# Kernel optimization log

Hardware: AMD Instinct MI355X
Metric: run time of the kernel (lower is better)

Reference implementation:

```python
import jax, jax.numpy as jnp
import numpy as np

B, C, N, K = 8, 256, 4096, 16

def setup_inputs() -> dict:
    key = jax.random.key(0)
    k1, k2, k3 = jax.random.split(key, 3)
    x = jax.random.normal(k1, (B, C, N, 1), dtype=jnp.float32)
    edge_index = jax.random.randint(k2, (2, B, N, K), 0, N, dtype=jnp.int64)
    eps = jnp.zeros((1,), dtype=jnp.float32)
    W = jax.random.normal(k3, (C, C), dtype=jnp.float32) * (1.0 / np.sqrt(C))
    b = jnp.zeros((C,), dtype=jnp.float32)
    return {"x": x, "edge_index": edge_index, "eps": eps, "W": W, "b": b}

def reference(x, edge_index, eps, W, b):
    # x: [B, C, N, 1]; edge_index: [2, B, N, K]
    idx = edge_index[0]                                  # [B, N, K] neighbor ids
    x_sq = x[..., 0]                                     # [B, C, N]
    # batched_index_select: gather neighbor features -> [B, C, N, K]
    gath = jnp.take_along_axis(
        x_sq, idx.reshape(B, 1, N * K).astype(jnp.int32), axis=2
    ).reshape(B, C, N, K)
    x_j = jnp.sum(gath, axis=-1, keepdims=True)          # [B, C, N, 1]
    h = (1.0 + eps[0]) * x + x_j                         # GIN update
    # BasicConv: 1x1 Conv2d + bias + ReLU
    out = jnp.einsum('oc,bcnk->bonk', W, h) + b[None, :, None, None]
    return jax.nn.relu(out)
```

## Files before the change

### kernel.cpp

```cpp
#include <hip/hip_runtime.h>
#include <stdint.h>

#define BB 8
#define CC 256
#define NN 4096
#define KK 16
#define NT 32

typedef float f32x4 __attribute__((ext_vector_type(4)));
typedef short bf16x8 __attribute__((ext_vector_type(8)));
typedef int   i32x4 __attribute__((ext_vector_type(4)));

__device__ __forceinline__ ushort f2bf(float f) {
  union { float f; uint32_t u; } v; v.f = f;
  uint32_t r = v.u + 0x7FFFu + ((v.u >> 16) & 1u);
  return (ushort)(r >> 16);
}
__device__ __forceinline__ float bf2f(ushort h) {
  union { uint32_t u; float f; } v; v.u = ((uint32_t)h) << 16;
  return v.f;
}

__global__ __launch_bounds__(256) void k_prep(
    const float* __restrict__ x, const float* __restrict__ W,
    ushort* __restrict__ xT, ushort* __restrict__ Wfrag)
{
  const int bid = blockIdx.x;
  const int t   = threadIdx.x;
  if (bid >= 2048) {
    const int wb = bid - 2048;
    const int o  = wb * 4 + (t >> 6);
    const int k0 = (t & 63) * 4;
    float4 v = *(const float4*)(W + (size_t)o * CC + k0);
    ushort4 h;
    h.x = f2bf(v.x); h.y = f2bf(v.y); h.z = f2bf(v.z); h.w = f2bf(v.w);
    const int kc = k0 >> 5, ks = k0 & 31;
    *(ushort4*)(Wfrag + ((size_t)(kc * CC + o)) * 32 + ks) = h;
    return;
  }
  __shared__ float tile[64][68];
  const int b    = bid & 7;
  const int tl   = bid >> 3;
  const int c0   = (tl & 3) * 64;
  const int n0   = (tl >> 2) * 64;
  {
    const int r  = t >> 2;
    const int cs = (t & 3) * 16;
    const float* xp = x + ((size_t)b * CC + c0 + r) * NN + n0 + cs;
    #pragma unroll
    for (int i = 0; i < 4; ++i) {
      float4 v = *(const float4*)(xp + i * 4);
      *(float4*)&tile[r][cs + i * 4] = v;
    }
  }
  __syncthreads();
  const int nl = t >> 2;
  const int cl = (t & 3) * 16;
  union { ushort s[16]; uint4 q[2]; } pk;
  #pragma unroll
  for (int i = 0; i < 16; ++i) pk.s[i] = f2bf(tile[cl + i][nl]);
  uint4* dst = (uint4*)(xT + ((size_t)b * NN + n0 + nl) * CC + c0 + cl);
  dst[0] = pk.q[0];
  dst[1] = pk.q[1];
}

__global__ __launch_bounds__(256) void k_fused(
    const ushort* __restrict__ xT, const int* __restrict__ edge0,
    const float* __restrict__ eps, const ushort* __restrict__ Wfrag,
    const float* __restrict__ bias, float* __restrict__ out)
{
  __shared__ ushort hLds[NT][264];
  const int bid = blockIdx.x;
  const int b   = bid & 7;
  const int n0  = (bid >> 3) * NT;
  const int t    = threadIdx.x;
  const int wave = t >> 6, lane = t & 63;
  const float epsv = 1.0f + eps[0];
  const ushort* xb = xT + (size_t)b * NN * CC;

  const int half = lane >> 5;
  const int cl   = (lane & 31) * 8;
  #pragma unroll
  for (int it = 0; it < 4; ++it) {
    const int nl = wave * 8 + it * 2 + half;
    const int n  = n0 + nl;
    bf16x8 sv = *(const bf16x8*)(xb + (size_t)n * CC + cl);
    float a[8];
    #pragma unroll
    for (int j = 0; j < 8; ++j) a[j] = bf2f((ushort)sv[j]) * epsv;
    const i32x4* epv = (const i32x4*)(edge0 + ((size_t)b * NN + n) * KK);
    i32x4 e0 = __builtin_nontemporal_load(epv + 0);
    i32x4 e1 = __builtin_nontemporal_load(epv + 1);
    i32x4 e2 = __builtin_nontemporal_load(epv + 2);
    i32x4 e3 = __builtin_nontemporal_load(epv + 3);
    const int js[16] = {e0.x, e0.y, e0.z, e0.w, e1.x, e1.y, e1.z, e1.w,
                        e2.x, e2.y, e2.z, e2.w, e3.x, e3.y, e3.z, e3.w};
    #pragma unroll
    for (int k = 0; k < KK; ++k) {
      bf16x8 g = *(const bf16x8*)(xb + (size_t)js[k] * CC + cl);
      #pragma unroll
      for (int j = 0; j < 8; ++j) a[j] += bf2f((ushort)g[j]);
    }
    union { ushort s[8]; bf16x8 v; } pk;
    #pragma unroll
    for (int j = 0; j < 8; ++j) pk.s[j] = f2bf(a[j]);
    *(bf16x8*)&hLds[nl][cl] = pk.v;
  }
  __syncthreads();

  f32x4 acc[4][NT / 16];
  #pragma unroll
  for (int m = 0; m < 4; ++m)
    #pragma unroll
    for (int nn = 0; nn < NT / 16; ++nn) acc[m][nn] = (f32x4){0.f, 0.f, 0.f, 0.f};

  const int lrow = lane & 15;
  const int kgrp = lane >> 4;
  const int o0   = wave * 64;

  #pragma unroll
  for (int kc = 0; kc < 8; ++kc) {
    const int cs = kgrp * 8;
    bf16x8 afr[4], bfr[NT / 16];
    #pragma unroll
    for (int m = 0; m < 4; ++m)
      afr[m] = *(const bf16x8*)(Wfrag +
          ((size_t)(kc * CC + o0 + m * 16 + lrow)) * 32 + cs);
    #pragma unroll
    for (int nn = 0; nn < NT / 16; ++nn)
      bfr[nn] = *(const bf16x8*)&hLds[nn * 16 + lrow][kc * 32 + cs];
    #pragma unroll
    for (int m = 0; m < 4; ++m)
      #pragma unroll
      for (int nn = 0; nn < NT / 16; ++nn)
        acc[m][nn] = __builtin_amdgcn_mfma_f32_16x16x32_bf16(
            afr[m], bfr[nn], acc[m][nn], 0, 0, 0);
  }

  #pragma unroll
  for (int m = 0; m < 4; ++m) {
    #pragma unroll
    for (int r = 0; r < 4; ++r) {
      const int o  = o0 + m * 16 + kgrp * 4 + r;
      const float bv = bias[o];
      #pragma unroll
      for (int nn = 0; nn < NT / 16; ++nn) {
        const int n = n0 + nn * 16 + lrow;
        float v = acc[m][nn][r] + bv;
        v = v > 0.f ? v : 0.f;
        __builtin_nontemporal_store(v, &out[((size_t)b * CC + o) * NN + n]);
      }
    }
  }
}

extern "C" void kernel_launch(void* const* d_in, const int* in_sizes, int n_in,
                              void* d_out, int out_size, void* d_ws, size_t ws_size,
                              hipStream_t stream) {
  const float* x    = (const float*)d_in[0];
  const int*   edge = (const int*)d_in[1];
  const float* eps  = (const float*)d_in[2];
  const float* W    = (const float*)d_in[3];
  const float* bias = (const float*)d_in[4];
  float* out = (float*)d_out;

  ushort* xT    = (ushort*)d_ws;
  ushort* Wfrag = xT + (size_t)BB * NN * CC;

  k_prep<<<2048 + 64, 256, 0, stream>>>(x, W, xT, Wfrag);

  k_fused<<<BB * (NN / NT), 256, 0, stream>>>(xT, edge, eps, Wfrag, bias, out);
}
```

Before: 121.1 us.

## Prefetch edge indices, use 32-bit offsets and packed bf16 unpack in gather

Edge indices for the next node are software-prefetched one iteration ahead, so the gather loads no longer wait on index loads. Gather addresses use 32-bit offsets, and bf16 pairs are unpacked with shift/mask into two f32x4 accumulators instead of per-element conversions. Also adds nontemporal loads in the prep kernel and a vectorised bias load. This adds register pressure from holding the prefetched indices, and the accumulation order changes slightly, with the self term now added after the neighbours.

After: 126.5 us. 4.5% more time.

```diff
diff --git a/kernel.cpp b/kernel.cpp
--- a/kernel.cpp
+++ b/kernel.cpp
@@ -10,15 +10,15 @@
 typedef float f32x4 __attribute__((ext_vector_type(4)));
 typedef short bf16x8 __attribute__((ext_vector_type(8)));
 typedef int   i32x4 __attribute__((ext_vector_type(4)));
+typedef unsigned int u32x4 __attribute__((ext_vector_type(4)));
 
 __device__ __forceinline__ ushort f2bf(float f) {
   union { float f; uint32_t u; } v; v.f = f;
   uint32_t r = v.u + 0x7FFFu + ((v.u >> 16) & 1u);
   return (ushort)(r >> 16);
 }
-__device__ __forceinline__ float bf2f(ushort h) {
-  union { uint32_t u; float f; } v; v.u = ((uint32_t)h) << 16;
-  return v.f;
+__device__ __forceinline__ float asf(uint32_t u) {
+  union { uint32_t u; float f; } v; v.u = u; return v.f;
 }
 
 __global__ __launch_bounds__(256) void k_prep(
@@ -31,7 +31,7 @@
     const int wb = bid - 2048;
     const int o  = wb * 4 + (t >> 6);
     const int k0 = (t & 63) * 4;
-    float4 v = *(const float4*)(W + (size_t)o * CC + k0);
+    f32x4 v = __builtin_nontemporal_load((const f32x4*)(W + (size_t)o * CC + k0));
     ushort4 h;
     h.x = f2bf(v.x); h.y = f2bf(v.y); h.z = f2bf(v.z); h.w = f2bf(v.w);
     const int kc = k0 >> 5, ks = k0 & 31;
@@ -49,8 +49,8 @@
     const float* xp = x + ((size_t)b * CC + c0 + r) * NN + n0 + cs;
     #pragma unroll
     for (int i = 0; i < 4; ++i) {
-      float4 v = *(const float4*)(xp + i * 4);
-      *(float4*)&tile[r][cs + i * 4] = v;
+      f32x4 v = __builtin_nontemporal_load((const f32x4*)(xp + i * 4));
+      *(f32x4*)&tile[r][cs + i * 4] = v;
     }
   }
   __syncthreads();
@@ -79,32 +79,64 @@
   const ushort* xb = xT + (size_t)b * NN * CC;
 
   const int half = lane >> 5;
-  const int cl   = (lane & 31) * 8;
+  const int co   = (lane & 31) * 8;
+  const uint32_t cb = (uint32_t)co;
+  const int* ep_base = edge0 + ((size_t)b * NN) * KK;
+
+  i32x4 e0, e1, e2, e3;
+  {
+    const i32x4* p = (const i32x4*)(ep_base + (size_t)(n0 + wave * 8 + half) * KK);
+    e0 = __builtin_nontemporal_load(p + 0);
+    e1 = __builtin_nontemporal_load(p + 1);
+    e2 = __builtin_nontemporal_load(p + 2);
+    e3 = __builtin_nontemporal_load(p + 3);
+  }
+
   #pragma unroll
   for (int it = 0; it < 4; ++it) {
     const int nl = wave * 8 + it * 2 + half;
     const int n  = n0 + nl;
-    bf16x8 sv = *(const bf16x8*)(xb + (size_t)n * CC + cl);
-    float a[8];
-    #pragma unroll
-    for (int j = 0; j < 8; ++j) a[j] = bf2f((ushort)sv[j]) * epsv;
-    const i32x4* epv = (const i32x4*)(edge0 + ((size_t)b * NN + n) * KK);
-    i32x4 e0 = __builtin_nontemporal_load(epv + 0);
-    i32x4 e1 = __builtin_nontemporal_load(epv + 1);
-    i32x4 e2 = __builtin_nontemporal_load(epv + 2);
-    i32x4 e3 = __builtin_nontemporal_load(epv + 3);
+    i32x4 f0, f1, f2, f3;
+    if (it < 3) {
+      const i32x4* p = (const i32x4*)(ep_base + (size_t)(n + 2) * KK);
+      f0 = __builtin_nontemporal_load(p + 0);
+      f1 = __builtin_nontemporal_load(p + 1);
+      f2 = __builtin_nontemporal_load(p + 2);
+      f3 = __builtin_nontemporal_load(p + 3);
+    }
+    const uint32_t soff = ((uint32_t)n << 8) + cb;
+    u32x4 sv = *(const u32x4*)(xb + soff);
+
+    f32x4 accL = (f32x4){0.f, 0.f, 0.f, 0.f};
+    f32x4 accH = (f32x4){0.f, 0.f, 0.f, 0.f};
     const int js[16] = {e0.x, e0.y, e0.z, e0.w, e1.x, e1.y, e1.z, e1.w,
                         e2.x, e2.y, e2.z, e2.w, e3.x, e3.y, e3.z, e3.w};
     #pragma unroll
     for (int k = 0; k < KK; ++k) {
-      bf16x8 g = *(const bf16x8*)(xb + (size_t)js[k] * CC + cl);
-      #pragma unroll
-      for (int j = 0; j < 8; ++j) a[j] += bf2f((ushort)g[j]);
-    }
-    union { ushort s[8]; bf16x8 v; } pk;
-    #pragma unroll
-    for (int j = 0; j < 8; ++j) pk.s[j] = f2bf(a[j]);
-    *(bf16x8*)&hLds[nl][cl] = pk.v;
+      const uint32_t off = ((uint32_t)js[k] << 8) + cb;
+      u32x4 g = *(const u32x4*)(xb + off);
+      f32x4 lo = (f32x4){asf(g.x << 16), asf(g.y << 16),
+                         asf(g.z << 16), asf(g.w << 16)};
+      f32x4 hi = (f32x4){asf(g.x & 0xffff0000u), asf(g.y & 0xffff0000u),
+                         asf(g.z & 0xffff0000u), asf(g.w & 0xffff0000u)};
+      accL += lo;
+      accH += hi;
+    }
+    f32x4 sL = (f32x4){asf(sv.x << 16), asf(sv.y << 16),
+                       asf(sv.z << 16), asf(sv.w << 16)};
+    f32x4 sH = (f32x4){asf(sv.x & 0xffff0000u), asf(sv.y & 0xffff0000u),
+                       asf(sv.z & 0xffff0000u), asf(sv.w & 0xffff0000u)};
+    accL += sL * epsv;
+    accH += sH * epsv;
+
+    u32x4 pk;
+    pk.x = (uint32_t)f2bf(accL[0]) | ((uint32_t)f2bf(accH[0]) << 16);
+    pk.y = (uint32_t)f2bf(accL[1]) | ((uint32_t)f2bf(accH[1]) << 16);
+    pk.z = (uint32_t)f2bf(accL[2]) | ((uint32_t)f2bf(accH[2]) << 16);
+    pk.w = (uint32_t)f2bf(accL[3]) | ((uint32_t)f2bf(accH[3]) << 16);
+    *(u32x4*)&hLds[nl][co] = pk;
+
+    e0 = f0; e1 = f1; e2 = f2; e3 = f3;
   }
   __syncthreads();
 
@@ -123,9 +155,10 @@
     const int cs = kgrp * 8;
     bf16x8 afr[4], bfr[NT / 16];
     #pragma unroll
-    for (int m = 0; m < 4; ++m)
-      afr[m] = *(const bf16x8*)(Wfrag +
-          ((size_t)(kc * CC + o0 + m * 16 + lrow)) * 32 + cs);
+    for (int m = 0; m < 4; ++m) {
+      const uint32_t aoff = (uint32_t)(kc * CC + o0 + m * 16 + lrow) * 32 + cs;
+      afr[m] = *(const bf16x8*)(Wfrag + aoff);
+    }
     #pragma unroll
     for (int nn = 0; nn < NT / 16; ++nn)
       bfr[nn] = *(const bf16x8*)&hLds[nn * 16 + lrow][kc * 32 + cs];
@@ -139,14 +172,14 @@
 
   #pragma unroll
   for (int m = 0; m < 4; ++m) {
+    const f32x4 bv4 = *(const f32x4*)(bias + o0 + m * 16 + kgrp * 4);
     #pragma unroll
     for (int r = 0; r < 4; ++r) {
       const int o  = o0 + m * 16 + kgrp * 4 + r;
-      const float bv = bias[o];
       #pragma unroll
       for (int nn = 0; nn < NT / 16; ++nn) {
         const int n = n0 + nn * 16 + lrow;
-        float v = acc[m][nn][r] + bv;
+        float v = acc[m][nn][r] + bv4[r];
         v = v > 0.f ? v : 0.f;
         __builtin_nontemporal_store(v, &out[((size_t)b * CC + o) * NN + n]);
       }
```

## Halve node tile and gather one node per wave with scalar neighbor indices

Applied to the files above, without the earlier changes.

Shrinks the per-block node tile from 32 to 16, doubling the grid. Each wave now gathers a whole node row, with every lane loading 4 bf16 channels, and the neighbor index is made wave-uniform through readfirstlane so row addressing runs on the scalar unit. The MFMA stage drops to one B fragment per wave, and bias is loaded as a vector. The aim is more parallelism and cheaper gather addressing, at the cost of reloading the W fragments twice as often per node and issuing narrower 8-byte gather loads.

New measurement: 143.7 us. 1.19x slower.

```diff
diff --git a/kernel.cpp b/kernel.cpp
--- a/kernel.cpp
+++ b/kernel.cpp
@@ -5,20 +5,21 @@
 #define CC 256
 #define NN 4096
 #define KK 16
-#define NT 32
+#define NT 16
 
 typedef float f32x4 __attribute__((ext_vector_type(4)));
 typedef short bf16x8 __attribute__((ext_vector_type(8)));
 typedef int   i32x4 __attribute__((ext_vector_type(4)));
+typedef unsigned int u32x2 __attribute__((ext_vector_type(2)));
+typedef unsigned int u32x4 __attribute__((ext_vector_type(4)));
 
 __device__ __forceinline__ ushort f2bf(float f) {
   union { float f; uint32_t u; } v; v.f = f;
   uint32_t r = v.u + 0x7FFFu + ((v.u >> 16) & 1u);
   return (ushort)(r >> 16);
 }
-__device__ __forceinline__ float bf2f(ushort h) {
-  union { uint32_t u; float f; } v; v.u = ((uint32_t)h) << 16;
-  return v.f;
+__device__ __forceinline__ float asf(uint32_t u) {
+  union { uint32_t u; float f; } v; v.u = u; return v.f;
 }
 
 __global__ __launch_bounds__(256) void k_prep(
@@ -31,7 +32,7 @@
     const int wb = bid - 2048;
     const int o  = wb * 4 + (t >> 6);
     const int k0 = (t & 63) * 4;
-    float4 v = *(const float4*)(W + (size_t)o * CC + k0);
+    f32x4 v = __builtin_nontemporal_load((const f32x4*)(W + (size_t)o * CC + k0));
     ushort4 h;
     h.x = f2bf(v.x); h.y = f2bf(v.y); h.z = f2bf(v.z); h.w = f2bf(v.w);
     const int kc = k0 >> 5, ks = k0 & 31;
@@ -49,8 +50,8 @@
     const float* xp = x + ((size_t)b * CC + c0 + r) * NN + n0 + cs;
     #pragma unroll
     for (int i = 0; i < 4; ++i) {
-      float4 v = *(const float4*)(xp + i * 4);
-      *(float4*)&tile[r][cs + i * 4] = v;
+      f32x4 v = __builtin_nontemporal_load((const f32x4*)(xp + i * 4));
+      *(f32x4*)&tile[r][cs + i * 4] = v;
     }
   }
   __syncthreads();
@@ -77,42 +78,43 @@
   const int wave = t >> 6, lane = t & 63;
   const float epsv = 1.0f + eps[0];
   const ushort* xb = xT + (size_t)b * NN * CC;
+  const int c4 = lane * 4;
 
-  const int half = lane >> 5;
-  const int cl   = (lane & 31) * 8;
   #pragma unroll
-  for (int it = 0; it < 4; ++it) {
-    const int nl = wave * 8 + it * 2 + half;
+  for (int i = 0; i < NT / 4; ++i) {
+    const int nl = wave * (NT / 4) + i;
     const int n  = n0 + nl;
-    bf16x8 sv = *(const bf16x8*)(xb + (size_t)n * CC + cl);
-    float a[8];
-    #pragma unroll
-    for (int j = 0; j < 8; ++j) a[j] = bf2f((ushort)sv[j]) * epsv;
     const i32x4* epv = (const i32x4*)(edge0 + ((size_t)b * NN + n) * KK);
     i32x4 e0 = __builtin_nontemporal_load(epv + 0);
     i32x4 e1 = __builtin_nontemporal_load(epv + 1);
     i32x4 e2 = __builtin_nontemporal_load(epv + 2);
     i32x4 e3 = __builtin_nontemporal_load(epv + 3);
+    u32x2 sv = *(const u32x2*)(xb + (n << 8) + c4);
+
     const int js[16] = {e0.x, e0.y, e0.z, e0.w, e1.x, e1.y, e1.z, e1.w,
                         e2.x, e2.y, e2.z, e2.w, e3.x, e3.y, e3.z, e3.w};
+    f32x4 acc = (f32x4){0.f, 0.f, 0.f, 0.f};
     #pragma unroll
     for (int k = 0; k < KK; ++k) {
-      bf16x8 g = *(const bf16x8*)(xb + (size_t)js[k] * CC + cl);
-      #pragma unroll
-      for (int j = 0; j < 8; ++j) a[j] += bf2f((ushort)g[j]);
+      const int jr = __builtin_amdgcn_readfirstlane(js[k]);
+      const ushort* rp = xb + ((size_t)jr << 8);
+      u32x2 g = *(const u32x2*)(rp + c4);
+      acc += (f32x4){asf(g.x << 16), asf(g.x & 0xffff0000u),
+                     asf(g.y << 16), asf(g.y & 0xffff0000u)};
     }
-    union { ushort s[8]; bf16x8 v; } pk;
-    #pragma unroll
-    for (int j = 0; j < 8; ++j) pk.s[j] = f2bf(a[j]);
-    *(bf16x8*)&hLds[nl][cl] = pk.v;
+    acc += (f32x4){asf(sv.x << 16), asf(sv.x & 0xffff0000u),
+                   asf(sv.y << 16), asf(sv.y & 0xffff0000u)} * epsv;
+
+    uint2 pk;
+    pk.x = (uint32_t)f2bf(acc[0]) | ((uint32_t)f2bf(acc[1]) << 16);
+    pk.y = (uint32_t)f2bf(acc[2]) | ((uint32_t)f2bf(acc[3]) << 16);
+    *(uint2*)&hLds[nl][c4] = pk;
   }
   __syncthreads();
 
-  f32x4 acc[4][NT / 16];
+  f32x4 acc2[4];
   #pragma unroll
-  for (int m = 0; m < 4; ++m)
-    #pragma unroll
-    for (int nn = 0; nn < NT / 16; ++nn) acc[m][nn] = (f32x4){0.f, 0.f, 0.f, 0.f};
+  for (int m = 0; m < 4; ++m) acc2[m] = (f32x4){0.f, 0.f, 0.f, 0.f};
 
   const int lrow = lane & 15;
   const int kgrp = lane >> 4;
@@ -121,35 +123,29 @@
   #pragma unroll
   for (int kc = 0; kc < 8; ++kc) {
     const int cs = kgrp * 8;
-    bf16x8 afr[4], bfr[NT / 16];
+    bf16x8 bfr = *(const bf16x8*)&hLds[lrow][kc * 32 + cs];
+    bf16x8 afr[4];
+    #pragma unroll
+    for (int m = 0; m < 4; ++m) {
+      const uint32_t aoff = (uint32_t)(kc * CC + o0 + m * 16 + lrow) * 32 + cs;
+      afr[m] = *(const bf16x8*)(Wfrag + aoff);
+    }
     #pragma unroll
     for (int m = 0; m < 4; ++m)
-      afr[m] = *(const bf16x8*)(Wfrag +
-          ((size_t)(kc * CC + o0 + m * 16 + lrow)) * 32 + cs);
-    #pragma unroll
-    for (int nn = 0; nn < NT / 16; ++nn)
-      bfr[nn] = *(const bf16x8*)&hLds[nn * 16 + lrow][kc * 32 + cs];
-    #pragma unroll
-    for (int m = 0; m < 4; ++m)
-      #pragma unroll
-      for (int nn = 0; nn < NT / 16; ++nn)
-        acc[m][nn] = __builtin_amdgcn_mfma_f32_16x16x32_bf16(
-            afr[m], bfr[nn], acc[m][nn], 0, 0, 0);
+      acc2[m] = __builtin_amdgcn_mfma_f32_16x16x32_bf16(
+          afr[m], bfr, acc2[m], 0, 0, 0);
   }
 
+  const int n = n0 + lrow;
   #pragma unroll
   for (int m = 0; m < 4; ++m) {
+    const f32x4 bv4 = *(const f32x4*)(bias + o0 + m * 16 + kgrp * 4);
     #pragma unroll
     for (int r = 0; r < 4; ++r) {
-      const int o  = o0 + m * 16 + kgrp * 4 + r;
-      const float bv = bias[o];
-      #pragma unroll
-      for (int nn = 0; nn < NT / 16; ++nn) {
-        const int n = n0 + nn * 16 + lrow;
-        float v = acc[m][nn][r] + bv;
-        v = v > 0.f ? v : 0.f;
-        __builtin_nontemporal_store(v, &out[((size_t)b * CC + o) * NN + n]);
-      }
+      const int o = o0 + m * 16 + kgrp * 4 + r;
+      float v = acc2[m][r] + bv4[r];
+      v = v > 0.f ? v : 0.f;
+      __builtin_nontemporal_store(v, &out[((size_t)b * CC + o) * NN + n]);
     }
   }
 }
```
